# Performance work log

Hardware: AMD Instinct MI355X
Metric: run time of the kernel (lower is better)

## Reference

```python
import jax, jax.numpy as jnp
import numpy as np

N_PATCHES = 4
PATCH = 64  # image_size // n_patches = 256 // 4
GROUPS = 32
EPS = 1e-5


def setup_inputs() -> dict:
    key = jax.random.key(0)
    k1, k2 = jax.random.split(key)
    x = jax.random.normal(k1, (8, 128, 256, 256), dtype=jnp.float32)
    y = jax.random.normal(k2, (8, 128, 256, 256), dtype=jnp.float32)
    # GroupNorm affine params (torch default init: weight=1, bias=0)
    weight = jnp.ones((128,), dtype=jnp.float32)
    bias = jnp.zeros((128,), dtype=jnp.float32)
    return {"x": x, "y": y, "weight": weight, "bias": bias}


def reference(x, y, weight, bias):
    b, c, h, w = x.shape
    n, p, g = N_PATCHES, PATCH, GROUPS
    cg = c // g
    # extract patches: (b, c, n, p, n, p) -> (b, i, j, c, hp, wp)
    xp = x.reshape(b, c, n, p, n, p).transpose(0, 2, 4, 1, 3, 5)
    yp = y.reshape(b, c, n, p, n, p).transpose(0, 2, 4, 1, 3, 5)
    # per-patch GroupNorm in float32 (GroupNorm.forward casts to float)
    xg = xp.astype(jnp.float32).reshape(b, n, n, g, cg, p, p)
    mean = xg.mean(axis=(4, 5, 6), keepdims=True)
    var = xg.var(axis=(4, 5, 6), keepdims=True)
    xn = (xg - mean) * jax.lax.rsqrt(var + EPS)
    xn = xn.reshape(b, n, n, c, p, p)
    xn = xn * weight[:, None, None] + bias[:, None, None]
    xn = xn.astype(x.dtype)
    # silu-gated scale, shift = 0
    out = xn * (1.0 + jax.nn.silu(yp))
    # reassemble: (b, i, j, c, hp, wp) -> (b, c, i, hp, j, wp) -> (b, c, H, W)
    out = out.transpose(0, 3, 1, 4, 2, 5).reshape(b, c, h, w)
    return out
```

## Files before the change

### kernel.cpp

```cpp
#include <hip/hip_runtime.h>


constexpr int CHANNELS = 128;
constexpr int HW = 256;
constexpr int NP = 4;
constexpr int P = 64;
constexpr int G = 32;
constexpr int CPG = CHANNELS / G;
constexpr float EPS = 1e-5f;

__global__ __launch_bounds__(512, 4)
void gn_patch_gate_kernel(const float* __restrict__ x,
                          const float* __restrict__ y,
                          const float* __restrict__ wgt,
                          const float* __restrict__ bvec,
                          float* __restrict__ out)
{
    const int bid = blockIdx.x;
    const int g  = bid & 31;
    const int pj = (bid >> 5) & 3;
    const int pi = (bid >> 7) & 3;
    const int b  = bid >> 9;
    const int tid = threadIdx.x;

    const unsigned cstride = HW * HW;
    const unsigned base =
        (((unsigned)b * CHANNELS + (unsigned)g * CPG) * HW + (unsigned)pi * P) * HW
        + (unsigned)pj * P;

    float4 xv[8];
    unsigned addr[8];
    float s = 0.f, ss = 0.f;
#pragma unroll
    for (int k = 0; k < 8; ++k) {
        const unsigned u  = (unsigned)tid + (unsigned)(k << 9);
        const unsigned cc = u >> 10;
        const unsigned r  = (u >> 4) & 63;
        const unsigned c4 = u & 15;
        const unsigned a  = base + cc * cstride + r * HW + (c4 << 2);
        addr[k] = a;
        const float4 v = *reinterpret_cast<const float4*>(x + a);
        xv[k] = v;
        s  += (v.x + v.y) + (v.z + v.w);
        ss += (v.x * v.x + v.y * v.y) + (v.z * v.z + v.w * v.w);
    }

#pragma unroll
    for (int off = 32; off; off >>= 1) {
        s  += __shfl_xor(s, off);
        ss += __shfl_xor(ss, off);
    }
    __shared__ float red[16];
    const int wv = tid >> 6;
    if ((tid & 63) == 0) { red[wv] = s; red[8 + wv] = ss; }
    __syncthreads();
    float ts = 0.f, tss = 0.f;
#pragma unroll
    for (int q = 0; q < 8; ++q) { ts += red[q]; tss += red[8 + q]; }

    const float inv_n = 1.0f / 16384.0f;
    const float mean = ts * inv_n;
    const float var  = fmaxf(tss * inv_n - mean * mean, 0.f);
    const float rstd = rsqrtf(var + EPS);

    float scl[CPG], sft[CPG];
#pragma unroll
    for (int cc = 0; cc < CPG; ++cc) {
        const float wc = wgt[g * CPG + cc];
        scl[cc] = wc * rstd;
        sft[cc] = bvec[g * CPG + cc] - mean * rstd * wc;
    }

#pragma unroll
    for (int k = 0; k < 8; ++k) {
        const unsigned u  = (unsigned)tid + (unsigned)(k << 9);
        const unsigned cc = u >> 10;
        const unsigned a  = addr[k];
        const float4 yv = *reinterpret_cast<const float4*>(y + a);
        float4 o;
        {
            const float xn = xv[k].x * scl[cc] + sft[cc];
            o.x = xn * (1.f + yv.x / (1.f + expf(-yv.x)));
        }
        {
            const float xn = xv[k].y * scl[cc] + sft[cc];
            o.y = xn * (1.f + yv.y / (1.f + expf(-yv.y)));
        }
        {
            const float xn = xv[k].z * scl[cc] + sft[cc];
            o.z = xn * (1.f + yv.z / (1.f + expf(-yv.z)));
        }
        {
            const float xn = xv[k].w * scl[cc] + sft[cc];
            o.w = xn * (1.f + yv.w / (1.f + expf(-yv.w)));
        }
        *reinterpret_cast<float4*>(out + a) = o;
    }
}

extern "C" void kernel_launch(void* const* d_in, const int* in_sizes, int n_in,
                              void* d_out, int out_size, void* d_ws, size_t ws_size,
                              hipStream_t stream) {
    const float* x    = (const float*)d_in[0];
    const float* y    = (const float*)d_in[1];
    const float* wgt  = (const float*)d_in[2];
    const float* bvec = (const float*)d_in[3];
    float* out = (float*)d_out;

    const int B = in_sizes[0] / (CHANNELS * HW * HW);
    const int nblocks = B * NP * NP * G;
    gn_patch_gate_kernel<<<dim3(nblocks), dim3(512), 0, stream>>>(x, y, wgt, bvec, out);
}
```

Baseline: 157.3 us.

## Stage x tile in LDS and use fast exp2/rcp for silu gate

Moves the per-block x tile from registers into a 64KB shared-memory buffer, so registers are freed, and recomputes addresses in the second pass. Replaces the expf plus divide in the silu gate with hardware exp2 and reciprocal intrinsics. The LDS footprint limits residency to about two blocks per CU, down from four, which may reduce latency hiding in this bandwidth-bound kernel. The fast intrinsics slightly reduce accuracy.

Result: faster. 153.1 us (-2.7%).

```diff
diff --git a/kernel.cpp b/kernel.cpp
--- a/kernel.cpp
+++ b/kernel.cpp
@@ -4,18 +4,25 @@
 constexpr int CHANNELS = 128;
 constexpr int HW = 256;
 constexpr int NP = 4;
-constexpr int P = 64;
 constexpr int G = 32;
 constexpr int CPG = CHANNELS / G;
 constexpr float EPS = 1e-5f;
 
-__global__ __launch_bounds__(512, 4)
+__device__ __forceinline__ float fast_gate(float v) {
+    const float e = __builtin_amdgcn_exp2f(v * -1.44269504088896f);
+    return 1.0f + v * __builtin_amdgcn_rcpf(1.0f + e);
+}
+
+__global__ __launch_bounds__(512, 2)
 void gn_patch_gate_kernel(const float* __restrict__ x,
                           const float* __restrict__ y,
                           const float* __restrict__ wgt,
                           const float* __restrict__ bvec,
                           float* __restrict__ out)
 {
+    __shared__ float4 xs[4096];
+    __shared__ float red[16];
+
     const int bid = blockIdx.x;
     const int g  = bid & 31;
     const int pj = (bid >> 5) & 3;
@@ -25,11 +32,9 @@
 
     const unsigned cstride = HW * HW;
     const unsigned base =
-        (((unsigned)b * CHANNELS + (unsigned)g * CPG) * HW + (unsigned)pi * P) * HW
-        + (unsigned)pj * P;
+        (((unsigned)b * CHANNELS + (unsigned)g * CPG) * HW + (unsigned)pi * 64) * HW
+        + (unsigned)pj * 64;
 
-    float4 xv[8];
-    unsigned addr[8];
     float s = 0.f, ss = 0.f;
 #pragma unroll
     for (int k = 0; k < 8; ++k) {
@@ -38,9 +43,8 @@
         const unsigned r  = (u >> 4) & 63;
         const unsigned c4 = u & 15;
         const unsigned a  = base + cc * cstride + r * HW + (c4 << 2);
-        addr[k] = a;
         const float4 v = *reinterpret_cast<const float4*>(x + a);
-        xv[k] = v;
+        xs[u] = v;
         s  += (v.x + v.y) + (v.z + v.w);
         ss += (v.x * v.x + v.y * v.y) + (v.z * v.z + v.w * v.w);
     }
@@ -50,7 +54,6 @@
         s  += __shfl_xor(s, off);
         ss += __shfl_xor(ss, off);
     }
-    __shared__ float red[16];
     const int wv = tid >> 6;
     if ((tid & 63) == 0) { red[wv] = s; red[8 + wv] = ss; }
     __syncthreads();
@@ -75,25 +78,16 @@
     for (int k = 0; k < 8; ++k) {
         const unsigned u  = (unsigned)tid + (unsigned)(k << 9);
         const unsigned cc = u >> 10;
-        const unsigned a  = addr[k];
+        const unsigned r  = (u >> 4) & 63;
+        const unsigned c4 = u & 15;
+        const unsigned a  = base + cc * cstride + r * HW + (c4 << 2);
         const float4 yv = *reinterpret_cast<const float4*>(y + a);
+        const float4 v  = xs[u];
         float4 o;
-        {
-            const float xn = xv[k].x * scl[cc] + sft[cc];
-            o.x = xn * (1.f + yv.x / (1.f + expf(-yv.x)));
-        }
-        {
-            const float xn = xv[k].y * scl[cc] + sft[cc];
-            o.y = xn * (1.f + yv.y / (1.f + expf(-yv.y)));
-        }
-        {
-            const float xn = xv[k].z * scl[cc] + sft[cc];
-            o.z = xn * (1.f + yv.z / (1.f + expf(-yv.z)));
-        }
-        {
-            const float xn = xv[k].w * scl[cc] + sft[cc];
-            o.w = xn * (1.f + yv.w / (1.f + expf(-yv.w)));
-        }
+        o.x = (v.x * scl[cc] + sft[cc]) * fast_gate(yv.x);
+        o.y = (v.y * scl[cc] + sft[cc]) * fast_gate(yv.y);
+        o.z = (v.z * scl[cc] + sft[cc]) * fast_gate(yv.z);
+        o.w = (v.w * scl[cc] + sft[cc]) * fast_gate(yv.w);
         *reinterpret_cast<float4*>(out + a) = o;
     }
 }
```
